# Performance work log

Measured on AMD Instinct MI355X. Metric: run time of the kernel, lower is better.

Reference implementation:

```python
import jax, jax.numpy as jnp
import numpy as np

N = 8192
D_IN = 32
HIDDEN = [32, 32, 32]   # -> 2 GraphConvolution layers
FC = [32, 1]            # hfc = [32, 32, 1] -> 2 Linear layers


def _uniform(key, shape, stdv):
    return jax.random.uniform(key, shape, jnp.float32, -stdv, stdv)


def setup_inputs() -> dict:
    key = jax.random.key(0)
    ks = jax.random.split(key, 32)
    inp = {}
    inp["V"] = jax.random.normal(ks[0], (N, D_IN), jnp.float32)
    inp["adj"] = jax.random.randint(ks[1], (N, N), 0, 4, jnp.int32)
    # GCN layer params: w1, w2, w3 [in, out], bias [out]; init U(-stdv, stdv), stdv = 1/sqrt(out)
    ki = 2
    for li in range(len(HIDDEN) - 1):
        a, b = HIDDEN[li], HIDDEN[li + 1]
        stdv = 1.0 / np.sqrt(b)
        for wname in ("w1", "w2", "w3"):
            inp[f"{wname}_{li}"] = _uniform(ks[ki], (a, b), stdv); ki += 1
        inp[f"gb_{li}"] = _uniform(ks[ki], (b,), stdv); ki += 1
    # FC params (torch Linear default init: U(-1/sqrt(in), 1/sqrt(in)))
    hfc = [HIDDEN[-1]] + FC
    for li in range(len(hfc) - 1):
        a, b = hfc[li], hfc[li + 1]
        stdv = 1.0 / np.sqrt(a)
        inp[f"fcW_{li}"] = _uniform(ks[ki], (b, a), stdv); ki += 1  # torch Linear weight is [out, in]
        inp[f"fcb_{li}"] = _uniform(ks[ki], (b,), stdv); ki += 1
    return inp


def _gcn(V, adj, w1, w2, w3, bias):
    # masked-adjacency relational aggregation: sum_k (adj==k) @ (V @ w_k)
    dt = V.dtype
    o = (adj == 1).astype(dt) @ (V @ w1)
    o = o + (adj == 2).astype(dt) @ (V @ w2)
    o = o + (adj == 3).astype(dt) @ (V @ w3)
    return jax.nn.relu(o + bias)


def reference(V, adj, w1_0, w2_0, w3_0, gb_0, w1_1, w2_1, w3_1, gb_1,
              fcW_0, fcb_0, fcW_1, fcb_1):
    Z = _gcn(V, adj, w1_0, w2_0, w3_0, gb_0)          # [N, 32]
    Z = _gcn(Z, adj, w1_1, w2_1, w3_1, gb_1)          # [N, 32]
    Z = jnp.sum(Z, axis=0)                             # [32] sum pooling over nodes
    Z = jax.nn.relu(Z @ fcW_0.T + fcb_0)               # dropout = identity (eval mode)
    Z = Z @ fcW_1.T + fcb_1                            # [1]
    return jax.nn.sigmoid(Z)
```

## Files before the change

### kernel.cpp

```cpp
#include <hip/hip_runtime.h>
#include <cmath>

#define NN 8192

typedef float floatx4 __attribute__((ext_vector_type(4)));
typedef unsigned int uint;
typedef unsigned long long u64;

template <int L2>
__global__ __launch_bounds__(256) void h_kernel(
    const float* __restrict__ X, const float* __restrict__ w1,
    const float* __restrict__ w2, const float* __restrict__ w3,
    const float* __restrict__ gbias, u64* __restrict__ Hfrag) {
  __shared__ float wl[32][32];
  __shared__ float Xs[64][32];
  const int tid = threadIdx.x;
  const int ch = blockIdx.y;
  const float* wsrc = (ch == 0) ? w1 : (ch == 1) ? w2 : w3;
  for (int i = tid; i < 1024; i += 256) ((float*)wl)[i] = wsrc[i];
  const size_t base = (size_t)blockIdx.x * 2048 + tid * 8;
  if (L2 == 0) {
    float4 x0 = ((const float4*)(X + base))[0];
    float4 x1 = ((const float4*)(X + base))[1];
    *((float4*)(&Xs[0][0] + tid * 8)) = x0;
    *((float4*)(&Xs[0][0] + tid * 8 + 4)) = x1;
  } else {
    float4 s0 = {0.f, 0.f, 0.f, 0.f}, s1 = {0.f, 0.f, 0.f, 0.f};
#pragma unroll
    for (int c = 0; c < 8; ++c) {
      const float4* p = (const float4*)(X + (size_t)c * NN * 32 + base);
      float4 a = p[0], b = p[1];
      s0.x += a.x; s0.y += a.y; s0.z += a.z; s0.w += a.w;
      s1.x += b.x; s1.y += b.y; s1.z += b.z; s1.w += b.w;
    }
    const int c0 = (tid * 8) & 31;
    const float4 b0 = *(const float4*)(gbias + c0);
    const float4 b1 = *(const float4*)(gbias + c0 + 4);
    s0.x += b0.x; s0.y += b0.y; s0.z += b0.z; s0.w += b0.w;
    s1.x += b1.x; s1.y += b1.y; s1.z += b1.z; s1.w += b1.w;
    s0.x = s0.x > 0.f ? s0.x : 0.f; s0.y = s0.y > 0.f ? s0.y : 0.f;
    s0.z = s0.z > 0.f ? s0.z : 0.f; s0.w = s0.w > 0.f ? s0.w : 0.f;
    s1.x = s1.x > 0.f ? s1.x : 0.f; s1.y = s1.y > 0.f ? s1.y : 0.f;
    s1.z = s1.z > 0.f ? s1.z : 0.f; s1.w = s1.w > 0.f ? s1.w : 0.f;
    *((float4*)(&Xs[0][0] + tid * 8)) = s0;
    *((float4*)(&Xs[0][0] + tid * 8 + 4)) = s1;
  }
  __syncthreads();
  const int n = tid & 31, jb = tid >> 5;
  const int j0 = blockIdx.x * 64 + jb * 8;
  const int t = j0 >> 5;
  const int lane = (n & 15) | (((j0 & 31) >> 3) << 4);
  const int tile = n >> 4;
  float av[8];
#pragma unroll
  for (int jj = 0; jj < 8; ++jj) {
    const float4* xr = (const float4*)(&Xs[jb * 8 + jj][0]);
    float acc = 0.f;
#pragma unroll
    for (int d4 = 0; d4 < 8; ++d4) {
      float4 x = xr[d4];
      acc += x.x * wl[d4 * 4 + 0][n];
      acc += x.y * wl[d4 * 4 + 1][n];
      acc += x.z * wl[d4 * 4 + 2][n];
      acc += x.w * wl[d4 * 4 + 3][n];
    }
    av[jj] = acc;
  }
  int lo = __builtin_amdgcn_cvt_pk_fp8_f32(av[0], av[1], 0, false);
  lo = __builtin_amdgcn_cvt_pk_fp8_f32(av[2], av[3], lo, true);
  int hi = __builtin_amdgcn_cvt_pk_fp8_f32(av[4], av[5], 0, false);
  hi = __builtin_amdgcn_cvt_pk_fp8_f32(av[6], av[7], hi, true);
  size_t idx = (((size_t)ch * 256 + t) * 2 + tile) * 64 + lane;
  Hfrag[idx] = ((u64)(uint)hi << 32) | (uint)(uint)lo;
}

#define BUILD_MASK(z, r0out, r1out)                                       \
  {                                                                       \
    const uint d0 = ((((z) & 0x55u) * 0x41041u) & 0x01010101u) << 6;      \
    const uint d1 = (((((z) >> 8) & 0x55u) * 0x41041u) & 0x01010101u)     \
                    << 6;                                                 \
    const uint d2 = (((((z) >> 16) & 0x55u) * 0x41041u) & 0x01010101u)    \
                    << 6;                                                 \
    const uint d3 = (((((z) >> 24) & 0x55u) * 0x41041u) & 0x01010101u)    \
                    << 6;                                                 \
    r0out = (long long)(((u64)d1 << 32) | d0);                            \
    r1out = (long long)(((u64)d3 << 32) | d2);                            \
  }

#define MF8(A, B, C) __builtin_amdgcn_mfma_f32_16x16x32_fp8_fp8((A), (B), (C), 0, 0, 0)

__device__ __forceinline__ void phaseB_core(const uint* mk,
                                            const u64* __restrict__ Hf,
                                            float* red_raw,
                                            float* __restrict__ Zpart, int rg,
                                            int c, int tid) {
  const int w = tid >> 6, lane = tid & 63;
  const int m = lane & 15, q = lane >> 4;
  const u64* hp = Hf + (size_t)(c * 32 + w * 8) * 128 + lane;
  long long b00 = hp[0],     b01 = hp[64];
  long long b10 = hp[32768], b11 = hp[32768 + 64];
  long long b20 = hp[65536], b21 = hp[65536 + 64];
  floatx4 acc00 = {0.f, 0.f, 0.f, 0.f}, acc01 = {0.f, 0.f, 0.f, 0.f};
  floatx4 acc10 = {0.f, 0.f, 0.f, 0.f}, acc11 = {0.f, 0.f, 0.f, 0.f};
#pragma unroll
  for (int tl = 0; tl < 8; ++tl) {
    long long n00, n01, n10, n11, n20, n21;
    if (tl < 7) {
      const u64* np = hp + (tl + 1) * 128;
      n00 = np[0];     n01 = np[64];
      n10 = np[32768]; n11 = np[32768 + 64];
      n20 = np[65536]; n21 = np[65536 + 64];
    }
    const uint pk = mk[tl];
    const uint x1 = pk ^ 0x55555555u;
    const uint z1 = ~(x1 | (x1 >> 1)) & 0x55555555u;
    const uint x2 = pk ^ 0xAAAAAAAAu;
    const uint z2 = ~(x2 | (x2 >> 1)) & 0x55555555u;
    const uint x3 = ~pk;
    const uint z3 = ~(x3 | (x3 >> 1)) & 0x55555555u;
    long long a1r0, a1r1, a2r0, a2r1, a3r0, a3r1;
    BUILD_MASK(z1, a1r0, a1r1);
    BUILD_MASK(z2, a2r0, a2r1);
    BUILD_MASK(z3, a3r0, a3r1);
    acc00 = MF8(a1r0, b00, acc00);
    acc00 = MF8(a2r0, b10, acc00);
    acc00 = MF8(a3r0, b20, acc00);
    acc01 = MF8(a1r0, b01, acc01);
    acc01 = MF8(a2r0, b11, acc01);
    acc01 = MF8(a3r0, b21, acc01);
    acc10 = MF8(a1r1, b00, acc10);
    acc10 = MF8(a2r1, b10, acc10);
    acc10 = MF8(a3r1, b20, acc10);
    acc11 = MF8(a1r1, b01, acc11);
    acc11 = MF8(a2r1, b11, acc11);
    acc11 = MF8(a3r1, b21, acc11);
    if (tl < 7) {
      b00 = n00; b01 = n01; b10 = n10; b11 = n11; b20 = n20; b21 = n21;
    }
  }
  float (*red)[4][64][4] = (float (*)[4][64][4])red_raw;
#pragma unroll
  for (int r = 0; r < 4; ++r) {
    red[w][0][lane][r] = acc00[r];
    red[w][1][lane][r] = acc01[r];
    red[w][2][lane][r] = acc10[r];
    red[w][3][lane][r] = acc11[r];
  }
  __syncthreads();
  if (w == 0) {
    const int rbase = rg * 32;
#pragma unroll
    for (int r = 0; r < 4; ++r) {
      const float c00 = 0.5f * (red[0][0][lane][r] + red[1][0][lane][r] +
                                red[2][0][lane][r] + red[3][0][lane][r]);
      const float c01 = 0.5f * (red[0][1][lane][r] + red[1][1][lane][r] +
                                red[2][1][lane][r] + red[3][1][lane][r]);
      const float c10 = 0.5f * (red[0][2][lane][r] + red[1][2][lane][r] +
                                red[2][2][lane][r] + red[3][2][lane][r]);
      const float c11 = 0.5f * (red[0][3][lane][r] + red[1][3][lane][r] +
                                red[2][3][lane][r] + red[3][3][lane][r]);
      const int ro0 = rbase + q * 4 + r;
      float* zp0 = Zpart + ((size_t)c * NN + ro0) * 32;
      zp0[m] = c00;
      zp0[16 + m] = c01;
      float* zp1 = Zpart + ((size_t)c * NN + ro0 + 16) * 32;
      zp1[m] = c10;
      zp1[16 + m] = c11;
    }
  }
}

__global__ __launch_bounds__(256, 4) void agg1_kernel(
    const int* __restrict__ adj, uint* __restrict__ packed_g,
    const u64* __restrict__ Hf, float* __restrict__ Zpart) {
  __shared__ char smraw[16384];
  uint* ptile = (uint*)smraw;
  const int tid = threadIdx.x;
  const int rg = blockIdx.x >> 3, c = blockIdx.x & 7;
  const int tg = tid >> 5;
  const int qt = (tid >> 1) & 3;
  const int t4 = (tid >> 3) & 3;
  const int ih = tid & 1;
  const int byte_base = tg * 1024 + qt * 256 + t4 * 4 + ih;
  unsigned char* pb = (unsigned char*)ptile;
  const size_t gofs = (size_t)rg * 32 * NN + c * 1024 + tid * 4;
#pragma unroll
  for (int r0 = 0; r0 < 32; r0 += 8) {
    int4 a[8];
#pragma unroll
    for (int rr = 0; rr < 8; ++rr)
      a[rr] = *(const int4*)(adj + gofs + (size_t)(r0 + rr) * NN);
#pragma unroll
    for (int rr = 0; rr < 8; ++rr) {
      const int r = r0 + rr;
      const uint b = (uint)(a[rr].x & 3) | ((uint)(a[rr].y & 3) << 2) |
                     ((uint)(a[rr].z & 3) << 4) | ((uint)(a[rr].w & 3) << 6);
      pb[byte_base + (r & 15) * 16 + (r >> 4) * 2] = (unsigned char)b;
    }
  }
  __syncthreads();
  uint* pg = packed_g + (size_t)blockIdx.x * 2048;
  *(uint4*)(pg + tid * 8) = *(const uint4*)(ptile + tid * 8);
  *(uint4*)(pg + tid * 8 + 4) = *(const uint4*)(ptile + tid * 8 + 4);
  const int w = tid >> 6, lane = tid & 63;
  uint mk[8];
  *(uint4*)(mk) = *(const uint4*)(ptile + (w * 2) * 256 + lane * 4);
  *(uint4*)(mk + 4) = *(const uint4*)(ptile + (w * 2 + 1) * 256 + lane * 4);
  __syncthreads();
  phaseB_core(mk, Hf, (float*)smraw, Zpart, rg, c, tid);
}

__global__ __launch_bounds__(256, 4) void agg2_kernel(
    const uint* __restrict__ packed_g, const u64* __restrict__ Hf,
    float* __restrict__ Zpart) {
  __shared__ float red_lds[4][4][64][4];
  const int tid = threadIdx.x;
  const int rg = blockIdx.x >> 3, c = blockIdx.x & 7;
  const int w = tid >> 6, lane = tid & 63;
  const uint* pg =
      packed_g + (size_t)blockIdx.x * 2048 + (w * 2) * 256 + lane * 4;
  uint mk[8];
  *(uint4*)(mk) = *(const uint4*)(pg);
  *(uint4*)(mk + 4) = *(const uint4*)(pg + 256);
  phaseB_core(mk, Hf, (float*)red_lds, Zpart, rg, c, tid);
}

__global__ __launch_bounds__(256) void pool_kernel(
    const float* __restrict__ Zpart, const float* __restrict__ bias,
    float* __restrict__ partials) {
  const int tid = threadIdx.x;
  const int col = tid & 31, ro = tid >> 5;
  const float b = bias[col];
  float s = 0.f;
  for (int rr = 0; rr < 32; ++rr) {
    const size_t r = (size_t)blockIdx.x * 256 + ro * 32 + rr;
    float v = b;
#pragma unroll
    for (int c = 0; c < 8; ++c) v += Zpart[(size_t)c * NN * 32 + r * 32 + col];
    s += v > 0.f ? v : 0.f;
  }
  __shared__ float red[8][32];
  red[ro][col] = s;
  __syncthreads();
  if (tid < 32) {
    float t = 0.f;
#pragma unroll
    for (int i = 0; i < 8; ++i) t += red[i][tid];
    partials[(size_t)blockIdx.x * 32 + tid] = t;
  }
}

__global__ __launch_bounds__(256) void fc_kernel(
    const float* __restrict__ partials, int np, const float* __restrict__ W0,
    const float* __restrict__ b0, const float* __restrict__ W1,
    const float* __restrict__ b1, float* __restrict__ out) {
  __shared__ float acc8[8][32];
  __shared__ float z[32], y[32];
  const int tid = threadIdx.x;
  const int col = tid & 31, ch = tid >> 5;
  float s = 0.f;
  for (int i = ch; i < np; i += 8) s += partials[(size_t)i * 32 + col];
  acc8[ch][col] = s;
  __syncthreads();
  if (tid < 32) {
    float t = 0.f;
#pragma unroll
    for (int i = 0; i < 8; ++i) t += acc8[i][tid];
    z[tid] = t;
  }
  __syncthreads();
  if (tid < 32) {
    float acc = b0[tid];
    for (int n = 0; n < 32; ++n) acc += W0[tid * 32 + n] * z[n];
    y[tid] = acc > 0.f ? acc : 0.f;
  }
  __syncthreads();
  if (tid == 0) {
    float acc = b1[0];
    for (int mm = 0; mm < 32; ++mm) acc += W1[mm] * y[mm];
    out[0] = 1.f / (1.f + expf(-acc));
  }
}

extern "C" void kernel_launch(void* const* d_in, const int* in_sizes, int n_in,
                              void* d_out, int out_size, void* d_ws,
                              size_t ws_size, hipStream_t stream) {
  const float* V   = (const float*)d_in[0];
  const int*   adj = (const int*)d_in[1];
  const float *w10 = (const float*)d_in[2], *w20 = (const float*)d_in[3],
              *w30 = (const float*)d_in[4], *gb0 = (const float*)d_in[5];
  const float *w11 = (const float*)d_in[6], *w21 = (const float*)d_in[7],
              *w31 = (const float*)d_in[8], *gb1 = (const float*)d_in[9];
  const float *fW0 = (const float*)d_in[10], *fb0 = (const float*)d_in[11],
              *fW1 = (const float*)d_in[12], *fb1 = (const float*)d_in[13];
  float* out = (float*)d_out;
  char* ws = (char*)d_ws;

  u64*   Hfrag    = (u64*)ws;
  float* Zpart    = (float*)(ws + 786432);
  float* partials = (float*)(ws + 9175040);
  uint*  packed   = (uint*)(ws + 9437184);

  h_kernel<0><<<dim3(128, 3), 256, 0, stream>>>(V, w10, w20, w30, nullptr,
                                                Hfrag);
  agg1_kernel<<<2048, 256, 0, stream>>>(adj, packed, Hfrag, Zpart);
  h_kernel<1><<<dim3(128, 3), 256, 0, stream>>>(Zpart, w11, w21, w31, gb0,
                                                Hfrag);
  agg2_kernel<<<2048, 256, 0, stream>>>(packed, Hfrag, Zpart);
  pool_kernel<<<32, 256, 0, stream>>>(Zpart, gb1, partials);
  fc_kernel<<<1, 256, 0, stream>>>(partials, 32, fW0, fb0, fW1, fb1, out);
}
```

Baseline: 421.7 us.

## Fuse column-chunk reduction, layer-2 projection and pooling into aggregation kernels

```diff
diff --git a/kernel.cpp b/kernel.cpp
--- a/kernel.cpp
+++ b/kernel.cpp
@@ -7,11 +7,10 @@
 typedef unsigned int uint;
 typedef unsigned long long u64;
 
-template <int L2>
 __global__ __launch_bounds__(256) void h_kernel(
     const float* __restrict__ X, const float* __restrict__ w1,
     const float* __restrict__ w2, const float* __restrict__ w3,
-    const float* __restrict__ gbias, u64* __restrict__ Hfrag) {
+    u64* __restrict__ Hfrag) {
   __shared__ float wl[32][32];
   __shared__ float Xs[64][32];
   const int tid = threadIdx.x;
@@ -19,32 +18,10 @@
   const float* wsrc = (ch == 0) ? w1 : (ch == 1) ? w2 : w3;
   for (int i = tid; i < 1024; i += 256) ((float*)wl)[i] = wsrc[i];
   const size_t base = (size_t)blockIdx.x * 2048 + tid * 8;
-  if (L2 == 0) {
-    float4 x0 = ((const float4*)(X + base))[0];
-    float4 x1 = ((const float4*)(X + base))[1];
-    *((float4*)(&Xs[0][0] + tid * 8)) = x0;
-    *((float4*)(&Xs[0][0] + tid * 8 + 4)) = x1;
-  } else {
-    float4 s0 = {0.f, 0.f, 0.f, 0.f}, s1 = {0.f, 0.f, 0.f, 0.f};
-#pragma unroll
-    for (int c = 0; c < 8; ++c) {
-      const float4* p = (const float4*)(X + (size_t)c * NN * 32 + base);
-      float4 a = p[0], b = p[1];
-      s0.x += a.x; s0.y += a.y; s0.z += a.z; s0.w += a.w;
-      s1.x += b.x; s1.y += b.y; s1.z += b.z; s1.w += b.w;
-    }
-    const int c0 = (tid * 8) & 31;
-    const float4 b0 = *(const float4*)(gbias + c0);
-    const float4 b1 = *(const float4*)(gbias + c0 + 4);
-    s0.x += b0.x; s0.y += b0.y; s0.z += b0.z; s0.w += b0.w;
-    s1.x += b1.x; s1.y += b1.y; s1.z += b1.z; s1.w += b1.w;
-    s0.x = s0.x > 0.f ? s0.x : 0.f; s0.y = s0.y > 0.f ? s0.y : 0.f;
-    s0.z = s0.z > 0.f ? s0.z : 0.f; s0.w = s0.w > 0.f ? s0.w : 0.f;
-    s1.x = s1.x > 0.f ? s1.x : 0.f; s1.y = s1.y > 0.f ? s1.y : 0.f;
-    s1.z = s1.z > 0.f ? s1.z : 0.f; s1.w = s1.w > 0.f ? s1.w : 0.f;
-    *((float4*)(&Xs[0][0] + tid * 8)) = s0;
-    *((float4*)(&Xs[0][0] + tid * 8 + 4)) = s1;
-  }
+  float4 x0 = ((const float4*)(X + base))[0];
+  float4 x1 = ((const float4*)(X + base))[1];
+  *((float4*)(&Xs[0][0] + tid * 8)) = x0;
+  *((float4*)(&Xs[0][0] + tid * 8 + 4)) = x1;
   __syncthreads();
   const int n = tid & 31, jb = tid >> 5;
   const int j0 = blockIdx.x * 64 + jb * 8;
@@ -89,27 +66,21 @@
 
 #define MF8(A, B, C) __builtin_amdgcn_mfma_f32_16x16x32_fp8_fp8((A), (B), (C), 0, 0, 0)
 
-__device__ __forceinline__ void phaseB_core(const uint* mk,
-                                            const u64* __restrict__ Hf,
-                                            float* red_raw,
-                                            float* __restrict__ Zpart, int rg,
-                                            int c, int tid) {
-  const int w = tid >> 6, lane = tid & 63;
-  const int m = lane & 15, q = lane >> 4;
-  const u64* hp = Hf + (size_t)(c * 32 + w * 8) * 128 + lane;
-  long long b00 = hp[0],     b01 = hp[64];
-  long long b10 = hp[32768], b11 = hp[32768 + 64];
-  long long b20 = hp[65536], b21 = hp[65536 + 64];
-  floatx4 acc00 = {0.f, 0.f, 0.f, 0.f}, acc01 = {0.f, 0.f, 0.f, 0.f};
-  floatx4 acc10 = {0.f, 0.f, 0.f, 0.f}, acc11 = {0.f, 0.f, 0.f, 0.f};
-#pragma unroll
-  for (int tl = 0; tl < 8; ++tl) {
+__device__ __forceinline__ void phaseB4(uint4 mkv, const u64* __restrict__ hp,
+                                        floatx4& acc00, floatx4& acc01,
+                                        floatx4& acc10, floatx4& acc11) {
+  uint mk[4] = {mkv.x, mkv.y, mkv.z, mkv.w};
+  long long b00 = (long long)hp[0],     b01 = (long long)hp[64];
+  long long b10 = (long long)hp[32768], b11 = (long long)hp[32768 + 64];
+  long long b20 = (long long)hp[65536], b21 = (long long)hp[65536 + 64];
+#pragma unroll
+  for (int tl = 0; tl < 4; ++tl) {
     long long n00, n01, n10, n11, n20, n21;
-    if (tl < 7) {
+    if (tl < 3) {
       const u64* np = hp + (tl + 1) * 128;
-      n00 = np[0];     n01 = np[64];
-      n10 = np[32768]; n11 = np[32768 + 64];
-      n20 = np[65536]; n21 = np[65536 + 64];
+      n00 = (long long)np[0];     n01 = (long long)np[64];
+      n10 = (long long)np[32768]; n11 = (long long)np[32768 + 64];
+      n20 = (long long)np[65536]; n21 = (long long)np[65536 + 64];
     }
     const uint pk = mk[tl];
     const uint x1 = pk ^ 0x55555555u;
@@ -134,11 +105,79 @@
     acc11 = MF8(a1r1, b01, acc11);
     acc11 = MF8(a2r1, b11, acc11);
     acc11 = MF8(a3r1, b21, acc11);
-    if (tl < 7) {
+    if (tl < 3) {
       b00 = n00; b01 = n01; b10 = n10; b11 = n11; b20 = n20; b21 = n21;
     }
   }
-  float (*red)[4][64][4] = (float (*)[4][64][4])red_raw;
+}
+
+__global__ __launch_bounds__(512, 2) void agg1_kernel(
+    const int* __restrict__ adj, uint* __restrict__ packed_g,
+    const u64* __restrict__ Hf1, u64* __restrict__ Hf2,
+    const float* __restrict__ w1, const float* __restrict__ w2,
+    const float* __restrict__ w3, const float* __restrict__ gb0) {
+  __shared__ __align__(16) char smraw[65536];
+  uint* pt0 = (uint*)smraw;
+  uint* pt1 = (uint*)(smraw + 8192);
+  float (*red)[4][64][4] = (float (*)[4][64][4])(smraw + 16384);
+  float* wl = (float*)(smraw + 49152);
+  float* Zs = (float*)smraw;
+  const int tid = threadIdx.x;
+  const int rg = blockIdx.x;
+  const int w = tid >> 6, lane = tid & 63;
+  for (int i = tid; i < 3072; i += 512) {
+    const int chw = i >> 10;
+    const float* wsrc = (chw == 0) ? w1 : (chw == 1) ? w2 : w3;
+    wl[i] = wsrc[i & 1023];
+  }
+  const int tid2 = tid & 255, rhalf = tid >> 8;
+  const int byte_base = (tid2 >> 5) * 1024 + ((tid2 >> 1) & 3) * 256 +
+                        ((tid2 >> 3) & 3) * 4 + (tid2 & 1);
+  const int* abase =
+      adj + (size_t)rg * 32 * NN + (size_t)rhalf * 16 * NN + tid2 * 4;
+  {
+    int4 a[16];
+#pragma unroll
+    for (int rr = 0; rr < 16; ++rr)
+      a[rr] = *(const int4*)(abase + (size_t)rr * NN);
+    unsigned char* pb = (unsigned char*)pt0;
+#pragma unroll
+    for (int rr = 0; rr < 16; ++rr) {
+      const int r = rhalf * 16 + rr;
+      const uint b = (uint)(a[rr].x & 3) | ((uint)(a[rr].y & 3) << 2) |
+                     ((uint)(a[rr].z & 3) << 4) | ((uint)(a[rr].w & 3) << 6);
+      pb[byte_base + (r & 15) * 16 + (r >> 4) * 2] = (unsigned char)b;
+    }
+  }
+  __syncthreads();
+  floatx4 acc00 = {0.f, 0.f, 0.f, 0.f}, acc01 = {0.f, 0.f, 0.f, 0.f};
+  floatx4 acc10 = {0.f, 0.f, 0.f, 0.f}, acc11 = {0.f, 0.f, 0.f, 0.f};
+  for (int c = 0; c < 8; ++c) {
+    uint* ptc = (c & 1) ? pt1 : pt0;
+    uint* ptn = (c & 1) ? pt0 : pt1;
+    int4 a[16];
+    if (c < 7) {
+#pragma unroll
+      for (int rr = 0; rr < 16; ++rr)
+        a[rr] = *(const int4*)(abase + (c + 1) * 1024 + (size_t)rr * NN);
+    }
+    uint* pg = packed_g + ((size_t)rg * 8 + c) * 2048;
+    *(uint4*)(pg + tid * 4) = *(const uint4*)(ptc + tid * 4);
+    const uint4 mkv = *(const uint4*)(ptc + w * 256 + lane * 4);
+    const u64* hp = Hf1 + (size_t)(c * 32 + w * 4) * 128 + lane;
+    phaseB4(mkv, hp, acc00, acc01, acc10, acc11);
+    if (c < 7) {
+      unsigned char* pb = (unsigned char*)ptn;
+#pragma unroll
+      for (int rr = 0; rr < 16; ++rr) {
+        const int r = rhalf * 16 + rr;
+        const uint b = (uint)(a[rr].x & 3) | ((uint)(a[rr].y & 3) << 2) |
+                       ((uint)(a[rr].z & 3) << 4) | ((uint)(a[rr].w & 3) << 6);
+        pb[byte_base + (r & 15) * 16 + (r >> 4) * 2] = (unsigned char)b;
+      }
+    }
+    __syncthreads();
+  }
 #pragma unroll
   for (int r = 0; r < 4; ++r) {
     red[w][0][lane][r] = acc00[r];
@@ -148,105 +187,107 @@
   }
   __syncthreads();
   if (w == 0) {
-    const int rbase = rg * 32;
+    const int m = lane & 15, q = lane >> 4;
 #pragma unroll
     for (int r = 0; r < 4; ++r) {
-      const float c00 = 0.5f * (red[0][0][lane][r] + red[1][0][lane][r] +
-                                red[2][0][lane][r] + red[3][0][lane][r]);
-      const float c01 = 0.5f * (red[0][1][lane][r] + red[1][1][lane][r] +
-                                red[2][1][lane][r] + red[3][1][lane][r]);
-      const float c10 = 0.5f * (red[0][2][lane][r] + red[1][2][lane][r] +
-                                red[2][2][lane][r] + red[3][2][lane][r]);
-      const float c11 = 0.5f * (red[0][3][lane][r] + red[1][3][lane][r] +
-                                red[2][3][lane][r] + red[3][3][lane][r]);
-      const int ro0 = rbase + q * 4 + r;
-      float* zp0 = Zpart + ((size_t)c * NN + ro0) * 32;
-      zp0[m] = c00;
-      zp0[16 + m] = c01;
-      float* zp1 = Zpart + ((size_t)c * NN + ro0 + 16) * 32;
-      zp1[m] = c10;
-      zp1[16 + m] = c11;
-    }
-  }
-}
-
-__global__ __launch_bounds__(256, 4) void agg1_kernel(
-    const int* __restrict__ adj, uint* __restrict__ packed_g,
-    const u64* __restrict__ Hf, float* __restrict__ Zpart) {
-  __shared__ char smraw[16384];
-  uint* ptile = (uint*)smraw;
+      float c00 = 0.f, c01 = 0.f, c10 = 0.f, c11 = 0.f;
+#pragma unroll
+      for (int i = 0; i < 8; ++i) {
+        c00 += red[i][0][lane][r];
+        c01 += red[i][1][lane][r];
+        c10 += red[i][2][lane][r];
+        c11 += red[i][3][lane][r];
+      }
+      const int ro = q * 4 + r;
+      float z00 = 0.5f * c00 + gb0[m];
+      float z01 = 0.5f * c01 + gb0[16 + m];
+      float z10 = 0.5f * c10 + gb0[m];
+      float z11 = 0.5f * c11 + gb0[16 + m];
+      z00 = z00 > 0.f ? z00 : 0.f;
+      z01 = z01 > 0.f ? z01 : 0.f;
+      z10 = z10 > 0.f ? z10 : 0.f;
+      z11 = z11 > 0.f ? z11 : 0.f;
+      Zs[ro * 33 + m] = z00;
+      Zs[ro * 33 + 16 + m] = z01;
+      Zs[(ro + 16) * 33 + m] = z10;
+      Zs[(ro + 16) * 33 + 16 + m] = z11;
+    }
+  }
+  __syncthreads();
+  if (tid < 384) {
+    const int chp = tid >> 7, rem = tid & 127;
+    const int tile = rem >> 6, l2 = rem & 63;
+    const int n = tile * 16 + (l2 & 15), j0 = (l2 >> 4) * 8;
+    const float* wc = wl + chp * 1024;
+    float av[8];
+#pragma unroll
+    for (int e = 0; e < 8; ++e) {
+      float acc = 0.f;
+      const float* zr = Zs + (j0 + e) * 33;
+#pragma unroll
+      for (int d = 0; d < 32; ++d) acc += zr[d] * wc[d * 32 + n];
+      av[e] = acc;
+    }
+    int lo = __builtin_amdgcn_cvt_pk_fp8_f32(av[0], av[1], 0, false);
+    lo = __builtin_amdgcn_cvt_pk_fp8_f32(av[2], av[3], lo, true);
+    int hi = __builtin_amdgcn_cvt_pk_fp8_f32(av[4], av[5], 0, false);
+    hi = __builtin_amdgcn_cvt_pk_fp8_f32(av[6], av[7], hi, true);
+    Hf2[(((size_t)chp * 256 + rg) * 2 + tile) * 64 + l2] =
+        ((u64)(uint)hi << 32) | (uint)(uint)lo;
+  }
+}
+
+__global__ __launch_bounds__(512, 2) void agg2_kernel(
+    const uint* __restrict__ packed_g, const u64* __restrict__ Hf2,
+    const float* __restrict__ gb1, float* __restrict__ partials) {
+  __shared__ float red[8][4][64][4];
   const int tid = threadIdx.x;
-  const int rg = blockIdx.x >> 3, c = blockIdx.x & 7;
-  const int tg = tid >> 5;
-  const int qt = (tid >> 1) & 3;
-  const int t4 = (tid >> 3) & 3;
-  const int ih = tid & 1;
-  const int byte_base = tg * 1024 + qt * 256 + t4 * 4 + ih;
-  unsigned char* pb = (unsigned char*)ptile;
-  const size_t gofs = (size_t)rg * 32 * NN + c * 1024 + tid * 4;
-#pragma unroll
-  for (int r0 = 0; r0 < 32; r0 += 8) {
-    int4 a[8];
-#pragma unroll
-    for (int rr = 0; rr < 8; ++rr)
-      a[rr] = *(const int4*)(adj + gofs + (size_t)(r0 + rr) * NN);
-#pragma unroll
-    for (int rr = 0; rr < 8; ++rr) {
-      const int r = r0 + rr;
-      const uint b = (uint)(a[rr].x & 3) | ((uint)(a[rr].y & 3) << 2) |
-                     ((uint)(a[rr].z & 3) << 4) | ((uint)(a[rr].w & 3) << 6);
-      pb[byte_base + (r & 15) * 16 + (r >> 4) * 2] = (unsigned char)b;
-    }
-  }
-  __syncthreads();
-  uint* pg = packed_g + (size_t)blockIdx.x * 2048;
-  *(uint4*)(pg + tid * 8) = *(const uint4*)(ptile + tid * 8);
-  *(uint4*)(pg + tid * 8 + 4) = *(const uint4*)(ptile + tid * 8 + 4);
+  const int rg = blockIdx.x;
   const int w = tid >> 6, lane = tid & 63;
-  uint mk[8];
-  *(uint4*)(mk) = *(const uint4*)(ptile + (w * 2) * 256 + lane * 4);
-  *(uint4*)(mk + 4) = *(const uint4*)(ptile + (w * 2 + 1) * 256 + lane * 4);
-  __syncthreads();
-  phaseB_core(mk, Hf, (float*)smraw, Zpart, rg, c, tid);
-}
-
-__global__ __launch_bounds__(256, 4) void agg2_kernel(
-    const uint* __restrict__ packed_g, const u64* __restrict__ Hf,
-    float* __restrict__ Zpart) {
-  __shared__ float red_lds[4][4][64][4];
-  const int tid = threadIdx.x;
-  const int rg = blockIdx.x >> 3, c = blockIdx.x & 7;
-  const int w = tid >> 6, lane = tid & 63;
-  const uint* pg =
-      packed_g + (size_t)blockIdx.x * 2048 + (w * 2) * 256 + lane * 4;
-  uint mk[8];
-  *(uint4*)(mk) = *(const uint4*)(pg);
-  *(uint4*)(mk + 4) = *(const uint4*)(pg + 256);
-  phaseB_core(mk, Hf, (float*)red_lds, Zpart, rg, c, tid);
-}
-
-__global__ __launch_bounds__(256) void pool_kernel(
-    const float* __restrict__ Zpart, const float* __restrict__ bias,
-    float* __restrict__ partials) {
-  const int tid = threadIdx.x;
-  const int col = tid & 31, ro = tid >> 5;
-  const float b = bias[col];
-  float s = 0.f;
-  for (int rr = 0; rr < 32; ++rr) {
-    const size_t r = (size_t)blockIdx.x * 256 + ro * 32 + rr;
-    float v = b;
-#pragma unroll
-    for (int c = 0; c < 8; ++c) v += Zpart[(size_t)c * NN * 32 + r * 32 + col];
-    s += v > 0.f ? v : 0.f;
-  }
-  __shared__ float red[8][32];
-  red[ro][col] = s;
-  __syncthreads();
-  if (tid < 32) {
-    float t = 0.f;
-#pragma unroll
-    for (int i = 0; i < 8; ++i) t += red[i][tid];
-    partials[(size_t)blockIdx.x * 32 + tid] = t;
+  floatx4 acc00 = {0.f, 0.f, 0.f, 0.f}, acc01 = {0.f, 0.f, 0.f, 0.f};
+  floatx4 acc10 = {0.f, 0.f, 0.f, 0.f}, acc11 = {0.f, 0.f, 0.f, 0.f};
+  const uint* pgb = packed_g + (size_t)rg * 8 * 2048 + w * 256 + lane * 4;
+  for (int c = 0; c < 8; ++c) {
+    const uint4 mkv = *(const uint4*)(pgb + c * 2048);
+    const u64* hp = Hf2 + (size_t)(c * 32 + w * 4) * 128 + lane;
+    phaseB4(mkv, hp, acc00, acc01, acc10, acc11);
+  }
+#pragma unroll
+  for (int r = 0; r < 4; ++r) {
+    red[w][0][lane][r] = acc00[r];
+    red[w][1][lane][r] = acc01[r];
+    red[w][2][lane][r] = acc10[r];
+    red[w][3][lane][r] = acc11[r];
+  }
+  __syncthreads();
+  if (w == 0) {
+    const int m = lane & 15;
+    float s0 = 0.f, s1 = 0.f;
+#pragma unroll
+    for (int r = 0; r < 4; ++r) {
+      float c00 = 0.f, c01 = 0.f, c10 = 0.f, c11 = 0.f;
+#pragma unroll
+      for (int i = 0; i < 8; ++i) {
+        c00 += red[i][0][lane][r];
+        c01 += red[i][1][lane][r];
+        c10 += red[i][2][lane][r];
+        c11 += red[i][3][lane][r];
+      }
+      float z00 = 0.5f * c00 + gb1[m];
+      float z01 = 0.5f * c01 + gb1[16 + m];
+      float z10 = 0.5f * c10 + gb1[m];
+      float z11 = 0.5f * c11 + gb1[16 + m];
+      s0 += (z00 > 0.f ? z00 : 0.f) + (z10 > 0.f ? z10 : 0.f);
+      s1 += (z01 > 0.f ? z01 : 0.f) + (z11 > 0.f ? z11 : 0.f);
+    }
+    s0 += __shfl_xor(s0, 16);
+    s0 += __shfl_xor(s0, 32);
+    s1 += __shfl_xor(s1, 16);
+    s1 += __shfl_xor(s1, 32);
+    if ((lane >> 4) == 0) {
+      partials[rg * 32 + m] = s0;
+      partials[rg * 32 + 16 + m] = s1;
+    }
   }
 }
 
@@ -296,17 +337,14 @@
   float* out = (float*)d_out;
   char* ws = (char*)d_ws;
 
-  u64*   Hfrag    = (u64*)ws;
-  float* Zpart    = (float*)(ws + 786432);
-  float* partials = (float*)(ws + 9175040);
-  uint*  packed   = (uint*)(ws + 9437184);
-
-  h_kernel<0><<<dim3(128, 3), 256, 0, stream>>>(V, w10, w20, w30, nullptr,
-                                                Hfrag);
-  agg1_kernel<<<2048, 256, 0, stream>>>(adj, packed, Hfrag, Zpart);
-  h_kernel<1><<<dim3(128, 3), 256, 0, stream>>>(Zpart, w11, w21, w31, gb0,
-                                                Hfrag);
-  agg2_kernel<<<2048, 256, 0, stream>>>(packed, Hfrag, Zpart);
-  pool_kernel<<<32, 256, 0, stream>>>(Zpart, gb1, partials);
-  fc_kernel<<<1, 256, 0, stream>>>(partials, 32, fW0, fb0, fW1, fb1, out);
-}
+  u64*   Hf1      = (u64*)ws;
+  u64*   Hf2      = (u64*)(ws + 786432);
+  uint*  packed   = (uint*)(ws + 1572864);
+  float* partials = (float*)(ws + 18350080);
+
+  h_kernel<<<dim3(128, 3), 256, 0, stream>>>(V, w10, w20, w30, Hf1);
+  agg1_kernel<<<256, 512, 0, stream>>>(adj, packed, Hf1, Hf2, w11, w21, w31,
+                                       gb0);
+  agg2_kernel<<<256, 512, 0, stream>>>(packed, Hf2, gb1, partials);
+  fc_kernel<<<1, 256, 0, stream>>>(partials, 256, fW0, fb0, fW1, fb1, out);
+}
```

Result: faster. 411.2 us, median of 2 (-2.5%).
